# Performance work log

Measured on AMD Instinct MI355X. Metric: run time of the kernel, lower is better.

## Reference

```python
import jax, jax.numpy as jnp
import numpy as np

H = 8            # heads actually used for the q/k/v split (256 = 8 * 32)
D = 32           # per-head dim
SCALE = 64 ** -0.5  # original code scales by init-arg dim_head**-0.5 (=64), not the actual split dim


def setup_inputs() -> dict:
    key = jax.random.key(0)
    ks = jax.random.split(key, 7)
    b, nq, nk, dim = 4, 2048, 2048, 256
    s = 1.0 / np.sqrt(dim).astype(np.float32)
    c2 = jax.random.normal(ks[0], (b, nk, dim), jnp.float32)
    c1 = jax.random.normal(ks[1], (b, nq, dim), jnp.float32)
    # weights stored as [in, out] so y = x @ W (equivalent to torch Linear)
    Wq = jax.random.normal(ks[2], (dim, dim), jnp.float32) * s
    Wk = jax.random.normal(ks[3], (dim, dim), jnp.float32) * s
    Wv = jax.random.normal(ks[4], (dim, dim), jnp.float32) * s
    Wo = jax.random.normal(ks[5], (dim, dim), jnp.float32) * s
    bo = jax.random.normal(ks[6], (dim,), jnp.float32) * 0.01
    return {"c2": c2, "c1": c1, "Wq": Wq, "Wk": Wk, "Wv": Wv, "Wo": Wo, "bo": bo}


def reference(c2, c1, Wq, Wk, Wv, Wo, bo):
    b, nq, dim = c1.shape
    nk = c2.shape[1]
    q = (c1 @ Wq).reshape(b, nq, H, D)   # queries from c1
    k = (c2 @ Wk).reshape(b, nk, H, D)   # keys from c2
    v = (c2 @ Wv).reshape(b, nk, H, D)   # values from c2
    dots = jnp.einsum('bqhd,bkhd->bhqk', q, k) * SCALE  # [b,H,nq,nk]
    attn = jax.nn.softmax(dots, axis=-1)
    out = jnp.einsum('bhqk,bkhd->bqhd', attn, v).reshape(b, nq, dim)
    return out @ Wo + bo  # to_out projection (dropout=0.0 -> identity)
```

## Files before the change

### kernel.cpp

```cpp
#include <hip/hip_runtime.h>
#include <hip/hip_bf16.h>

typedef __bf16 bf16;
typedef __bf16 bf16x4 __attribute__((ext_vector_type(4)));
typedef __bf16 bf16x8 __attribute__((ext_vector_type(8)));
typedef float f32x4 __attribute__((ext_vector_type(4)));

#define MFMA(a, b, c) __builtin_amdgcn_mfma_f32_16x16x32_bf16(a, b, c, 0, 0, 0)

#define QSCALE (0.125f * 1.44269504088896340736f)

#define OFF_Q  262144
#define OFF_K  (OFF_Q + 2097152)
#define OFF_VT (OFF_K + 2097152)
#define OFF_P  (OFF_VT + 2097152)
#define OFF_L  (OFF_P + 4194304)

static __device__ __forceinline__ float fexp2(float x) {
    return __builtin_amdgcn_exp2f(x);
}

#define GLL16(g, l)                                                              \
    __builtin_amdgcn_global_load_lds(                                            \
        (const __attribute__((address_space(1))) void*)(g),                      \
        (__attribute__((address_space(3))) void*)(l), 16, 0, 0)

__global__ __launch_bounds__(256) void k_wt(const float* __restrict__ Wq,
                                            const float* __restrict__ Wk,
                                            const float* __restrict__ Wv,
                                            const float* __restrict__ Wo,
                                            bf16* __restrict__ wts) {
    int mat = blockIdx.y;
    const float* src = (mat == 0) ? Wq : (mat == 1) ? Wk : (mat == 2) ? Wv : Wo;
    int o = blockIdx.x;
    int i = threadIdx.x;
    wts[(size_t)mat * 65536 + o * 256 + i] = (bf16)src[i * 256 + o];
}

__global__ __launch_bounds__(64) void k_proj(const float* __restrict__ c1,
                                             const float* __restrict__ c2,
                                             const bf16* __restrict__ wts,
                                             bf16* __restrict__ qkv) {
    int m = blockIdx.x, nh = blockIdx.y, mat = blockIdx.z;
    const float* src = (mat == 0) ? c1 : c2;
    const bf16* wt = wts + (size_t)mat * 65536;
    int l = threadIdx.x;
    int cc = l & 15, g = l >> 4;
    int arow = m * 16 + cc;

    f32x4 acc[8] = {};
    if (mat != 2) {
#pragma unroll
        for (int kc = 0; kc < 8; ++kc) {
            const float* ap = src + (size_t)arow * 256 + kc * 32 + g * 8;
            f32x4 a0 = *reinterpret_cast<const f32x4*>(ap);
            f32x4 a1 = *reinterpret_cast<const f32x4*>(ap + 4);
            bf16x8 af;
#pragma unroll
            for (int j = 0; j < 4; ++j) {
                af[j] = (bf16)a0[j];
                af[j + 4] = (bf16)a1[j];
            }
#pragma unroll
            for (int ct = 0; ct < 8; ++ct) {
                bf16x8 bf = *reinterpret_cast<const bf16x8*>(
                    wt + (size_t)(nh * 128 + ct * 16 + cc) * 256 + kc * 32 + g * 8);
                acc[ct] = MFMA(af, bf, acc[ct]);
            }
        }
        float oscale = (mat == 0) ? QSCALE : 1.0f;
        bf16* dst = qkv + (size_t)mat * 2097152;
#pragma unroll
        for (int ct = 0; ct < 8; ++ct) {
            int col = nh * 128 + ct * 16 + cc;
#pragma unroll
            for (int j = 0; j < 4; ++j) {
                int grow = m * 16 + 4 * g + j;
                bf16 val = (bf16)(acc[ct][j] * oscale);
                int b = grow >> 11, n = grow & 2047;
                int h = col >> 5, d = col & 31;
                dst[(((size_t)(b * 8 + h)) * 2048 + n) * 32 + d] = val;
            }
        }
    } else {
#pragma unroll
        for (int kc = 0; kc < 8; ++kc) {
            const float* ap = src + (size_t)arow * 256 + kc * 32 + g * 8;
            f32x4 a0 = *reinterpret_cast<const f32x4*>(ap);
            f32x4 a1 = *reinterpret_cast<const f32x4*>(ap + 4);
            bf16x8 af;
#pragma unroll
            for (int j = 0; j < 4; ++j) {
                af[j] = (bf16)a0[j];
                af[j + 4] = (bf16)a1[j];
            }
#pragma unroll
            for (int ct = 0; ct < 8; ++ct) {
                bf16x8 bf = *reinterpret_cast<const bf16x8*>(
                    wt + (size_t)(nh * 128 + ct * 16 + cc) * 256 + kc * 32 + g * 8);
                acc[ct] = MFMA(bf, af, acc[ct]);
            }
        }
        bf16* vt = qkv + (size_t)2 * 2097152;
        int b = (m * 16) >> 11, n0 = (m * 16) & 2047;
#pragma unroll
        for (int ct = 0; ct < 8; ++ct) {
#pragma unroll
            for (int j = 0; j < 4; ++j) {
                vt[((size_t)b * 256 + nh * 128 + ct * 16 + 4 * g + j) * 2048 + n0 + cc] =
                    (bf16)acc[ct][j];
            }
        }
    }
}

__global__ __launch_bounds__(256, 4) void k_attn(const bf16* __restrict__ Q,
                                                 const bf16* __restrict__ K,
                                                 const bf16* __restrict__ Vt,
                                                 bf16* __restrict__ P,
                                                 float* __restrict__ Lf) {
    __shared__ __align__(16) bf16 sK[4][2048];
    __shared__ __align__(16) bf16 sV[4][2048];

    int flat = blockIdx.x;
    int xcd = flat & 7;
    int sub = flat >> 3;
    int bh = xcd * 4 + (sub & 3);
    int rest = sub >> 2;
    int xtile = rest & 15;
    int split = rest >> 4;

    int b = bh >> 3, hd = bh & 7;
    int kv0 = split << 10;
    int lane = threadIdx.x & 63;
    int w = threadIdx.x >> 6;
    int cc = lane & 15, g = lane >> 4;
    int qrow0 = xtile * 128 + w * 32;

    const bf16* Qh = Q + (size_t)bh * 65536;
    const bf16* Kh = K + (size_t)bh * 65536;
    const bf16* Vth = Vt + (size_t)bh * 65536;

    bf16x8 qf[2];
#pragma unroll
    for (int h = 0; h < 2; ++h)
        qf[h] = *reinterpret_cast<const bf16x8*>(
            Qh + (size_t)(qrow0 + h * 16 + cc) * 32 + g * 8);

    int kp0 = 8 * (cc >> 2) + (cc & 3);
    int kperm[4];
#pragma unroll
    for (int r = 0; r < 4; ++r) kperm[r] = 32 * (r >> 1) + 4 * (r & 1) + kp0;

    int dv = w * 8 + (lane >> 3);
    int vcol = ((lane & 7) ^ (lane >> 3)) * 8;

    float lsum[2] = {0.f, 0.f};
    f32x4 oA[2] = {}, oB[2] = {};

#define STAGE(t, buf)                                                           \
    do {                                                                        \
        int kb_ = kv0 + (t) * 64;                                               \
        const bf16* kg_ = Kh + (size_t)kb_ * 32 + w * 512 + lane * 8;           \
        GLL16(kg_, &sK[buf][w * 512]);                                          \
        const bf16* vg_ = Vth + (size_t)dv * 2048 + kb_ + vcol;                 \
        GLL16(vg_, &sV[buf][w * 512]);                                          \
    } while (0)

    STAGE(0, 0);
    STAGE(1, 1);

    for (int kt = 0; kt < 16; ++kt) {
        int cur = kt & 3;
        if (kt + 2 < 16) STAGE(kt + 2, (kt + 2) & 3);

        asm volatile("s_waitcnt vmcnt(4)" ::: "memory");
        __builtin_amdgcn_s_barrier();
        __builtin_amdgcn_sched_barrier(0);

        bf16x8 kf[4], vf[4];
#pragma unroll
        for (int r = 0; r < 4; ++r)
            kf[r] = *reinterpret_cast<const bf16x8*>(&sK[cur][kperm[r] * 32 + g * 8]);
#pragma unroll
        for (int dt = 0; dt < 2; ++dt)
#pragma unroll
            for (int kk = 0; kk < 2; ++kk) {
                int colp = (kk * 4 + g) ^ (cc & 7);
                vf[dt * 2 + kk] = *reinterpret_cast<const bf16x8*>(
                    &sV[cur][(dt * 16 + cc) * 64 + colp * 8]);
            }

#pragma unroll
        for (int h = 0; h < 2; ++h) {
            f32x4 z = {};
            f32x4 s[4];
            __builtin_amdgcn_s_setprio(1);
#pragma unroll
            for (int r = 0; r < 4; ++r) s[r] = MFMA(kf[r], qf[h], z);
            __builtin_amdgcn_s_setprio(0);

#pragma unroll
            for (int r = 0; r < 4; ++r)
#pragma unroll
                for (int j = 0; j < 4; ++j) s[r][j] = fexp2(s[r][j]);
            float t0 = (s[0][0] + s[0][1]) + (s[0][2] + s[0][3]);
            float t1 = (s[1][0] + s[1][1]) + (s[1][2] + s[1][3]);
            float t2 = (s[2][0] + s[2][1]) + (s[2][2] + s[2][3]);
            float t3 = (s[3][0] + s[3][1]) + (s[3][2] + s[3][3]);
            lsum[h] += (t0 + t1) + (t2 + t3);

            bf16x8 pb[2];
#pragma unroll
            for (int kk = 0; kk < 2; ++kk)
#pragma unroll
                for (int e = 0; e < 8; ++e)
                    pb[kk][e] = (bf16)s[2 * kk + (e >> 2)][e & 3];

            __builtin_amdgcn_s_setprio(1);
            oA[h] = MFMA(vf[0], pb[0], oA[h]);
            oA[h] = MFMA(vf[1], pb[1], oA[h]);
            oB[h] = MFMA(vf[2], pb[0], oB[h]);
            oB[h] = MFMA(vf[3], pb[1], oB[h]);
            __builtin_amdgcn_s_setprio(0);
        }
    }
#undef STAGE

#pragma unroll
    for (int h = 0; h < 2; ++h) {
        lsum[h] += __shfl_xor(lsum[h], 16);
        lsum[h] += __shfl_xor(lsum[h], 32);

        bf16* Pp = P + (size_t)split * 2097152 +
                   ((size_t)b * 2048 + qrow0 + h * 16 + cc) * 256 + hd * 32;
        bf16x4 w0, w1;
#pragma unroll
        for (int j = 0; j < 4; ++j) {
            w0[j] = (bf16)oA[h][j];
            w1[j] = (bf16)oB[h][j];
        }
        *reinterpret_cast<bf16x4*>(Pp + 4 * g) = w0;
        *reinterpret_cast<bf16x4*>(Pp + 16 + 4 * g) = w1;
        if (g == 0)
            Lf[(size_t)split * 65536 + (size_t)bh * 2048 + qrow0 + h * 16 + cc] = lsum[h];
    }
}

__global__ __launch_bounds__(64) void k_out(const bf16* __restrict__ P,
                                            const float* __restrict__ Lf,
                                            const bf16* __restrict__ WoT,
                                            const float* __restrict__ bo,
                                            float* __restrict__ out) {
    int m = blockIdx.x, nb = blockIdx.y;
    int l = threadIdx.x;
    int cc = l & 15, g = l >> 4;
    int arow = m * 16 + cc;
    int b = arow >> 11, n = arow & 2047;

    f32x4 acc[4] = {};
#pragma unroll
    for (int kc = 0; kc < 8; ++kc) {
        float l0 = Lf[(size_t)(b * 8 + kc) * 2048 + n];
        float l1 = Lf[65536 + (size_t)(b * 8 + kc) * 2048 + n];
        float inv = 1.0f / (l0 + l1);
        bf16x8 p0 = *reinterpret_cast<const bf16x8*>(
            P + (size_t)arow * 256 + kc * 32 + g * 8);
        bf16x8 p1 = *reinterpret_cast<const bf16x8*>(
            P + 2097152 + (size_t)arow * 256 + kc * 32 + g * 8);
        bf16x8 af;
#pragma unroll
        for (int e = 0; e < 8; ++e)
            af[e] = (bf16)(((float)p0[e] + (float)p1[e]) * inv);
#pragma unroll
        for (int ct = 0; ct < 4; ++ct) {
            bf16x8 bf = *reinterpret_cast<const bf16x8*>(
                WoT + (size_t)(nb * 64 + ct * 16 + cc) * 256 + kc * 32 + g * 8);
            acc[ct] = MFMA(af, bf, acc[ct]);
        }
    }
#pragma unroll
    for (int ct = 0; ct < 4; ++ct) {
        int col = nb * 64 + ct * 16 + cc;
        float bias = bo[col];
#pragma unroll
        for (int j = 0; j < 4; ++j) {
            int row = m * 16 + 4 * g + j;
            out[(size_t)row * 256 + col] = acc[ct][j] + bias;
        }
    }
}

extern "C" void kernel_launch(void* const* d_in, const int* in_sizes, int n_in,
                              void* d_out, int out_size, void* d_ws, size_t ws_size,
                              hipStream_t stream) {
    const float* c2 = (const float*)d_in[0];
    const float* c1 = (const float*)d_in[1];
    const float* Wq = (const float*)d_in[2];
    const float* Wk = (const float*)d_in[3];
    const float* Wv = (const float*)d_in[4];
    const float* Wo = (const float*)d_in[5];
    const float* bo = (const float*)d_in[6];
    float* out = (float*)d_out;

    bf16* ws = (bf16*)d_ws;
    bf16* wts = ws;
    bf16* Q = ws + OFF_Q;
    bf16* Vt = ws + OFF_VT;
    bf16* P = ws + OFF_P;
    float* Lf = (float*)(ws + OFF_L);

    k_wt<<<dim3(256, 4), 256, 0, stream>>>(Wq, Wk, Wv, Wo, wts);
    k_proj<<<dim3(512, 2, 3), 64, 0, stream>>>(c1, c2, wts, Q);
    k_attn<<<dim3(1024), 256, 0, stream>>>(Q, ws + OFF_K, Vt, P, Lf);
    k_out<<<dim3(512, 4), 64, 0, stream>>>(P, Lf, wts + 3 * 65536, bo, out);
}
```

Baseline: 81.84 us.

## Tile weight transpose, stage projection inputs in LDS, store Q/K row-major

Result: no change. 81.24 us (-0.7%).

```diff
diff --git a/kernel.cpp b/kernel.cpp
--- a/kernel.cpp
+++ b/kernel.cpp
@@ -30,86 +30,117 @@
                                             const float* __restrict__ Wv,
                                             const float* __restrict__ Wo,
                                             bf16* __restrict__ wts) {
-    int mat = blockIdx.y;
+    __shared__ __align__(16) bf16 tile[64][64];
+    int rb = blockIdx.x, ob = blockIdx.y, mat = blockIdx.z;
     const float* src = (mat == 0) ? Wq : (mat == 1) ? Wk : (mat == 2) ? Wv : Wo;
-    int o = blockIdx.x;
-    int i = threadIdx.x;
-    wts[(size_t)mat * 65536 + o * 256 + i] = (bf16)src[i * 256 + o];
-}
-
-__global__ __launch_bounds__(64) void k_proj(const float* __restrict__ c1,
-                                             const float* __restrict__ c2,
-                                             const bf16* __restrict__ wts,
-                                             bf16* __restrict__ qkv) {
-    int m = blockIdx.x, nh = blockIdx.y, mat = blockIdx.z;
-    const float* src = (mat == 0) ? c1 : c2;
+    int t = threadIdx.x;
+    int lr = t >> 4, lc = (t & 15) * 4;
+#pragma unroll
+    for (int rr = 0; rr < 4; ++rr) {
+        int i = rb * 64 + rr * 16 + lr;
+        f32x4 a = *reinterpret_cast<const f32x4*>(src + (size_t)i * 256 + ob * 64 + lc);
+        bf16x4 v;
+#pragma unroll
+        for (int j = 0; j < 4; ++j) v[j] = (bf16)a[j];
+        *reinterpret_cast<bf16x4*>(&tile[rr * 16 + lr][lc]) = v;
+    }
+    __syncthreads();
+    int ol = t >> 2, ib = (t & 3) * 16;
+    int o = ob * 64 + ol;
+    bf16x8 v0, v1;
+#pragma unroll
+    for (int k = 0; k < 8; ++k) {
+        v0[k] = tile[ib + k][ol];
+        v1[k] = tile[ib + 8 + k][ol];
+    }
+    bf16* dst = wts + (size_t)mat * 65536 + (size_t)o * 256 + rb * 64 + ib;
+    *reinterpret_cast<bf16x8*>(dst) = v0;
+    *reinterpret_cast<bf16x8*>(dst + 8) = v1;
+}
+
+__global__ __launch_bounds__(384) void k_proj(const float* __restrict__ c1,
+                                              const float* __restrict__ c2,
+                                              const bf16* __restrict__ wts,
+                                              bf16* __restrict__ qkv) {
+    __shared__ __align__(16) bf16 sA[2][4096];
+    int m = blockIdx.x;
+    int t = threadIdx.x;
+
+    if (t < 256) {
+        int row = t >> 4, c0t = t & 15;
+        const float* ap = c1 + ((size_t)m * 16 + row) * 256 + c0t * 16;
+        f32x4 a0 = *reinterpret_cast<const f32x4*>(ap);
+        f32x4 a1 = *reinterpret_cast<const f32x4*>(ap + 4);
+        f32x4 a2 = *reinterpret_cast<const f32x4*>(ap + 8);
+        f32x4 a3 = *reinterpret_cast<const f32x4*>(ap + 12);
+        bf16x8 w0, w1;
+#pragma unroll
+        for (int j = 0; j < 4; ++j) {
+            w0[j] = (bf16)a0[j]; w0[j + 4] = (bf16)a1[j];
+            w1[j] = (bf16)a2[j]; w1[j + 4] = (bf16)a3[j];
+        }
+        int kc = c0t >> 1, gA = (c0t & 1) * 2;
+        *reinterpret_cast<bf16x8*>(&sA[0][kc * 512 + (gA * 16 + row) * 8]) = w0;
+        *reinterpret_cast<bf16x8*>(&sA[0][kc * 512 + ((gA + 1) * 16 + row) * 8]) = w1;
+    }
+    if (t >= 128) {
+        int t2 = t - 128;
+        int row = t2 >> 4, c0t = t2 & 15;
+        const float* ap = c2 + ((size_t)m * 16 + row) * 256 + c0t * 16;
+        f32x4 a0 = *reinterpret_cast<const f32x4*>(ap);
+        f32x4 a1 = *reinterpret_cast<const f32x4*>(ap + 4);
+        f32x4 a2 = *reinterpret_cast<const f32x4*>(ap + 8);
+        f32x4 a3 = *reinterpret_cast<const f32x4*>(ap + 12);
+        bf16x8 w0, w1;
+#pragma unroll
+        for (int j = 0; j < 4; ++j) {
+            w0[j] = (bf16)a0[j]; w0[j + 4] = (bf16)a1[j];
+            w1[j] = (bf16)a2[j]; w1[j + 4] = (bf16)a3[j];
+        }
+        int kc = c0t >> 1, gA = (c0t & 1) * 2;
+        *reinterpret_cast<bf16x8*>(&sA[1][kc * 512 + (gA * 16 + row) * 8]) = w0;
+        *reinterpret_cast<bf16x8*>(&sA[1][kc * 512 + ((gA + 1) * 16 + row) * 8]) = w1;
+    }
+    __syncthreads();
+
+    int u = t >> 6;
+    int lane = t & 63, cc = lane & 15, g = lane >> 4;
+    int mat = u >> 1, nh = u & 1;
     const bf16* wt = wts + (size_t)mat * 65536;
-    int l = threadIdx.x;
-    int cc = l & 15, g = l >> 4;
-    int arow = m * 16 + cc;
+    const bf16* sAp = sA[mat == 0 ? 0 : 1];
 
     f32x4 acc[8] = {};
+#pragma unroll
+    for (int kc = 0; kc < 8; ++kc) {
+        bf16x8 af = *reinterpret_cast<const bf16x8*>(&sAp[kc * 512 + lane * 8]);
+#pragma unroll
+        for (int ct = 0; ct < 8; ++ct) {
+            bf16x8 bf = *reinterpret_cast<const bf16x8*>(
+                wt + (size_t)(nh * 128 + ct * 16 + cc) * 256 + kc * 32 + g * 8);
+            acc[ct] = (mat == 2) ? MFMA(bf, af, acc[ct])
+                                 : MFMA(af, bf, acc[ct]);
+        }
+    }
+
     if (mat != 2) {
-#pragma unroll
-        for (int kc = 0; kc < 8; ++kc) {
-            const float* ap = src + (size_t)arow * 256 + kc * 32 + g * 8;
-            f32x4 a0 = *reinterpret_cast<const f32x4*>(ap);
-            f32x4 a1 = *reinterpret_cast<const f32x4*>(ap + 4);
-            bf16x8 af;
-#pragma unroll
-            for (int j = 0; j < 4; ++j) {
-                af[j] = (bf16)a0[j];
-                af[j + 4] = (bf16)a1[j];
-            }
-#pragma unroll
-            for (int ct = 0; ct < 8; ++ct) {
-                bf16x8 bf = *reinterpret_cast<const bf16x8*>(
-                    wt + (size_t)(nh * 128 + ct * 16 + cc) * 256 + kc * 32 + g * 8);
-                acc[ct] = MFMA(af, bf, acc[ct]);
-            }
-        }
-        float oscale = (mat == 0) ? QSCALE : 1.0f;
+        float os = (mat == 0) ? QSCALE : 1.0f;
         bf16* dst = qkv + (size_t)mat * 2097152;
 #pragma unroll
         for (int ct = 0; ct < 8; ++ct) {
             int col = nh * 128 + ct * 16 + cc;
 #pragma unroll
-            for (int j = 0; j < 4; ++j) {
-                int grow = m * 16 + 4 * g + j;
-                bf16 val = (bf16)(acc[ct][j] * oscale);
-                int b = grow >> 11, n = grow & 2047;
-                int h = col >> 5, d = col & 31;
-                dst[(((size_t)(b * 8 + h)) * 2048 + n) * 32 + d] = val;
-            }
+            for (int j = 0; j < 4; ++j)
+                dst[(size_t)(m * 16 + 4 * g + j) * 256 + col] = (bf16)(acc[ct][j] * os);
         }
     } else {
-#pragma unroll
-        for (int kc = 0; kc < 8; ++kc) {
-            const float* ap = src + (size_t)arow * 256 + kc * 32 + g * 8;
-            f32x4 a0 = *reinterpret_cast<const f32x4*>(ap);
-            f32x4 a1 = *reinterpret_cast<const f32x4*>(ap + 4);
-            bf16x8 af;
-#pragma unroll
-            for (int j = 0; j < 4; ++j) {
-                af[j] = (bf16)a0[j];
-                af[j + 4] = (bf16)a1[j];
-            }
-#pragma unroll
-            for (int ct = 0; ct < 8; ++ct) {
-                bf16x8 bf = *reinterpret_cast<const bf16x8*>(
-                    wt + (size_t)(nh * 128 + ct * 16 + cc) * 256 + kc * 32 + g * 8);
-                acc[ct] = MFMA(bf, af, acc[ct]);
-            }
-        }
         bf16* vt = qkv + (size_t)2 * 2097152;
         int b = (m * 16) >> 11, n0 = (m * 16) & 2047;
 #pragma unroll
         for (int ct = 0; ct < 8; ++ct) {
 #pragma unroll
-            for (int j = 0; j < 4; ++j) {
+            for (int j = 0; j < 4; ++j)
                 vt[((size_t)b * 256 + nh * 128 + ct * 16 + 4 * g + j) * 2048 + n0 + cc] =
                     (bf16)acc[ct][j];
-            }
         }
     }
 }
@@ -137,21 +168,23 @@
     int cc = lane & 15, g = lane >> 4;
     int qrow0 = xtile * 128 + w * 32;
 
-    const bf16* Qh = Q + (size_t)bh * 65536;
-    const bf16* Kh = K + (size_t)bh * 65536;
+    const bf16* Qh = Q + (size_t)(b * 2048) * 256 + hd * 32;
     const bf16* Vth = Vt + (size_t)bh * 65536;
+    size_t kbase0 = (size_t)(b * 2048) * 256 + hd * 32;
 
     bf16x8 qf[2];
 #pragma unroll
     for (int h = 0; h < 2; ++h)
         qf[h] = *reinterpret_cast<const bf16x8*>(
-            Qh + (size_t)(qrow0 + h * 16 + cc) * 32 + g * 8);
+            Qh + (size_t)(qrow0 + h * 16 + cc) * 256 + g * 8);
 
     int kp0 = 8 * (cc >> 2) + (cc & 3);
     int kperm[4];
 #pragma unroll
     for (int r = 0; r < 4; ++r) kperm[r] = 32 * (r >> 1) + 4 * (r & 1) + kp0;
 
+    int krow = w * 16 + (lane >> 2);
+    int kcol = (lane & 3) * 8;
     int dv = w * 8 + (lane >> 3);
     int vcol = ((lane & 7) ^ (lane >> 3)) * 8;
 
@@ -161,7 +194,7 @@
 #define STAGE(t, buf)                                                           \
     do {                                                                        \
         int kb_ = kv0 + (t) * 64;                                               \
-        const bf16* kg_ = Kh + (size_t)kb_ * 32 + w * 512 + lane * 8;           \
+        const bf16* kg_ = K + kbase0 + (size_t)(kb_ + krow) * 256 + kcol;       \
         GLL16(kg_, &sK[buf][w * 512]);                                          \
         const bf16* vg_ = Vth + (size_t)dv * 2048 + kb_ + vcol;                 \
         GLL16(vg_, &sV[buf][w * 512]);                                          \
@@ -310,8 +343,8 @@
     bf16* P = ws + OFF_P;
     float* Lf = (float*)(ws + OFF_L);
 
-    k_wt<<<dim3(256, 4), 256, 0, stream>>>(Wq, Wk, Wv, Wo, wts);
-    k_proj<<<dim3(512, 2, 3), 64, 0, stream>>>(c1, c2, wts, Q);
+    k_wt<<<dim3(4, 4, 4), 256, 0, stream>>>(Wq, Wk, Wv, Wo, wts);
+    k_proj<<<dim3(512), 384, 0, stream>>>(c1, c2, wts, Q);
     k_attn<<<dim3(1024), 256, 0, stream>>>(Q, ws + OFF_K, Vt, P, Lf);
     k_out<<<dim3(512, 4), 64, 0, stream>>>(P, Lf, wts + 3 * 65536, bo, out);
 }
```
